# Kernel tuning notes

Hardware: AMD Instinct MI355X
Metric: run time of the kernel (lower is better)

## Reference

```python
import jax, jax.numpy as jnp
import numpy as np
from jax import lax

B = 256; D_IN = 2048; HID = 2048; NSEG = 10; D_CTX = 1024; OUT = 100; NI = 205
KW_PCT = 0.05
K = int(round(KW_PCT * HID))  # 102 winners per sample per layer
W_DENSITY = 0.05      # weight_sparsity = 0.95
DEND_DENSITY = 0.05   # dendrite_weight_sparsity = 0.95


def setup_inputs() -> dict:
    key = jax.random.key(0)
    ks = jax.random.split(key, 16)
    def u(k, shape, bound):
        return jax.random.uniform(k, shape, minval=-bound, maxval=bound, dtype=jnp.float32)
    inp = {}
    inp["x"] = jax.random.normal(ks[0], (B, D_IN), jnp.float32)
    inp["context"] = jax.random.normal(ks[1], (B, D_CTX), jnp.float32)
    # layer 1 FF weights: modified kaiming, input density 1.0 -> bound = 1/sqrt(fan_in)
    inp["W1"] = u(ks[2], (HID, D_IN), 1.0 / np.sqrt(D_IN))
    inp["b1"] = jnp.zeros((HID,), jnp.float32)
    # dendrites: input density 1.0 (context_percent_on=1), weight density 0.05
    dend_bound = 1.0 / np.sqrt(DEND_DENSITY * D_CTX)
    inp["segW1"] = u(ks[3], (HID, NSEG, D_CTX), dend_bound)
    inp["maskW1"] = (jax.random.uniform(ks[4], (HID, D_IN)) < W_DENSITY).astype(jnp.float32)
    inp["maskS1"] = (jax.random.uniform(ks[5], (HID, NSEG, D_CTX)) < DEND_DENSITY).astype(jnp.float32)
    # layer 2 FF weights: input density = kw_percent_on (k-winners upstream)
    inp["W2"] = u(ks[6], (HID, HID), 1.0 / np.sqrt(KW_PCT * HID))
    inp["b2"] = jnp.zeros((HID,), jnp.float32)
    inp["segW2"] = u(ks[7], (HID, NSEG, D_CTX), dend_bound)
    inp["maskW2"] = (jax.random.uniform(ks[8], (HID, HID)) < W_DENSITY).astype(jnp.float32)
    inp["maskS2"] = (jax.random.uniform(ks[9], (HID, NSEG, D_CTX)) < DEND_DENSITY).astype(jnp.float32)
    # Dale (EiDense) output head: non-negative excitatory/inhibitory factors
    s = 1.0 / np.sqrt(HID)
    inp["Wex_out"] = jax.random.uniform(ks[10], (OUT, HID), dtype=jnp.float32) * s
    inp["Wix_out"] = jax.random.uniform(ks[11], (1, HID), dtype=jnp.float32) * s
    inp["Wei_out"] = jax.random.uniform(ks[12], (OUT, 1), dtype=jnp.float32)
    inp["b_out"] = jnp.zeros((OUT,), jnp.float32)
    return inp


def _kwinners(y, k):
    # keep top-k activations per row, zero the rest (boost_strength=0)
    vals, idxs = lax.top_k(y, k)  # [B, k]
    rows = jnp.arange(y.shape[0])[:, None]
    return jnp.zeros_like(y).at[rows, idxs].set(vals)


def _dendritic_layer(x, context, W, b, segW, maskW, maskS):
    # sparse-masked feedforward projection
    y = x @ (W * maskW).T + b  # [B, HID]
    # per-unit dendrite segment activations from context
    d = jnp.einsum('bc,usc->bus', context, segW * maskS)  # [B, HID, NSEG]
    # absolute-max gating: pick segment with max |activation|, gate by sigmoid
    sel = jnp.argmax(jnp.abs(d), axis=-1)  # [B, HID]
    chosen = jnp.take_along_axis(d, sel[..., None], axis=-1)[..., 0]
    y = y * jax.nn.sigmoid(chosen)
    return _kwinners(y, K)


def reference(x, context, W1, b1, segW1, maskW1, maskS1, W2, b2, segW2, maskW2, maskS2, Wex_out, Wix_out, Wei_out, b_out):
    h = _dendritic_layer(x, context, W1, b1, segW1, maskW1, maskS1)
    h = _dendritic_layer(h, context, W2, b2, segW2, maskW2, maskS2)
    # EiDense output head: W = Wex - Wei @ Wix (Dale's law), no output nonlinearity
    W_out = Wex_out - Wei_out @ Wix_out  # [OUT, HID]
    return h @ W_out.T + b_out
```

## Files before the change

kernel.cpp:

```cpp
#include <hip/hip_runtime.h>
#include <math.h>

#define B_SZ   256
#define D_IN   2048
#define HID    2048
#define NSEG   10
#define D_CTX  1024
#define OUT_N  100
#define KWIN   102
#define CAPS   128

typedef float f32x4 __attribute__((ext_vector_type(4)));

__device__ __forceinline__ f32x4 ntld4(const float* p) {
  return __builtin_nontemporal_load((const f32x4*)p);
}

__device__ __forceinline__ unsigned f2key(float f) {
  unsigned b = __float_as_uint(f);
  return (b & 0x80000000u) ? ~b : (b | 0x80000000u);
}
__device__ __forceinline__ float key2f(unsigned k) {
  return (k & 0x80000000u) ? __uint_as_float(k & 0x7FFFFFFFu) : __uint_as_float(~k);
}

__global__ __launch_bounds__(256) void transpose2_k(const float* __restrict__ xsrc,
                                                    float* __restrict__ xdst,
                                                    const float* __restrict__ csrc,
                                                    float* __restrict__ cdst) {
  __shared__ float tile[32][33];
  int bid = blockIdx.x;
  const float* src; float* dst; int cols;
  const int NX = (D_IN / 32) * (B_SZ / 32);
  if (bid < NX) { src = xsrc; dst = xdst; cols = D_IN; }
  else { bid -= NX; src = csrc; dst = cdst; cols = D_CTX; }
  int nbx = cols / 32;
  int bx = bid % nbx, by = bid / nbx;
  int c0 = bx * 32, r0 = by * 32;
  int tx = threadIdx.x & 31, ty = threadIdx.x >> 5;
  for (int i = ty; i < 32; i += 8)
    tile[i][tx] = src[(r0 + i) * cols + (c0 + tx)];
  __syncthreads();
  for (int i = ty; i < 32; i += 8)
    dst[(c0 + i) * B_SZ + (r0 + tx)] = tile[tx][i];
}

__device__ __forceinline__ int compact_pairs_1024(const float* __restrict__ wrow,
                                                  const float* __restrict__ mrow,
                                                  int coff, float2* pairs) {
  const int t = threadIdx.x & 63;
  const unsigned long long below = (1ull << t) - 1ull;
  __builtin_amdgcn_wave_barrier();
  int base = 0;
#pragma unroll
  for (int i = 0; i < 4; ++i) {
    const int e = t + 64 * i;
    f32x4 ww = ntld4(wrow + 4 * e);
    f32x4 mm = ntld4(mrow + 4 * e);
    const float wv[4] = {ww.x, ww.y, ww.z, ww.w};
    const float mv[4] = {mm.x, mm.y, mm.z, mm.w};
    const int c = (e << 2) + coff;
#pragma unroll
    for (int j = 0; j < 4; ++j) {
      bool nz = (mv[j] != 0.f);
      unsigned long long bal = __ballot(nz);
      if (nz) {
        int pos = base + (int)__popcll(bal & below);
        if (pos < CAPS) pairs[pos] = make_float2(wv[j], __int_as_float(c + j));
      }
      base += (int)__popcll(bal);
    }
  }
  __builtin_amdgcn_wave_barrier();
  return base > CAPS ? CAPS : base;
}

__device__ __forceinline__ void gather_dot(const float* __restrict__ src,
                                           const float2* pairs, int cnt,
                                           int t4, float out4[4]) {
  float acc[4][4];
#pragma unroll
  for (int s = 0; s < 4; ++s)
#pragma unroll
    for (int i = 0; i < 4; ++i) acc[s][i] = 0.f;
  int j = 0;
  for (; j + 8 <= cnt; j += 8) {
#pragma unroll
    for (int s = 0; s < 8; ++s) {
      float2 p = pairs[j + s];
      const f32x4 cv = *(const f32x4*)(src + (__float_as_int(p.y) << 8) + t4);
      acc[s & 3][0] += cv.x * p.x; acc[s & 3][1] += cv.y * p.x;
      acc[s & 3][2] += cv.z * p.x; acc[s & 3][3] += cv.w * p.x;
    }
  }
  for (; j < cnt; ++j) {
    float2 p = pairs[j];
    const f32x4 cv = *(const f32x4*)(src + (__float_as_int(p.y) << 8) + t4);
    acc[0][0] += cv.x * p.x; acc[0][1] += cv.y * p.x;
    acc[0][2] += cv.z * p.x; acc[0][3] += cv.w * p.x;
  }
#pragma unroll
  for (int i = 0; i < 4; ++i)
    out4[i] = (acc[0][i] + acc[1][i]) + (acc[2][i] + acc[3][i]);
}

__global__ __launch_bounds__(256, 4) void dendff_kernel(
    const float* __restrict__ W1, const float* __restrict__ maskW1, const float* __restrict__ b1,
    const float* __restrict__ segW1, const float* __restrict__ maskS1,
    const float* __restrict__ segW2, const float* __restrict__ maskS2,
    const float* __restrict__ xT, const float* __restrict__ ctxT,
    float* __restrict__ y1T, float* __restrict__ gate2T) {
  __shared__ float2 pairs_s[4][CAPS];
  __shared__ float exch[2][64][13];
  const int wave = threadIdx.x >> 6;
  const int t = threadIdx.x & 63, t4 = t * 4;
  const int pidx = wave >> 1;
  const int half = wave & 1;
  const int row = blockIdx.x * 2 + pidx;
  const bool isL1 = (row < HID);
  const int u = isL1 ? row : (row - HID);
  const float* segW = (isL1 ? segW1 : segW2)
                      + (size_t)u * NSEG * D_CTX + (size_t)half * 5 * D_CTX;
  const float* maskS = (isL1 ? maskS1 : maskS2)
                      + (size_t)u * NSEG * D_CTX + (size_t)half * 5 * D_CTX;
  float2* pairs = pairs_s[wave];

  float bestA[4] = {-1.f, -1.f, -1.f, -1.f};
  float chosen[4] = {0.f, 0.f, 0.f, 0.f};

#pragma unroll 1
  for (int s = 0; s < 5; ++s) {
    int cnt = compact_pairs_1024(segW + s * D_CTX, maskS + s * D_CTX, 0, pairs);
    float d[4];
    gather_dot(ctxT, pairs, cnt, t4, d);
#pragma unroll
    for (int i = 0; i < 4; ++i) {
      float a = fabsf(d[i]);
      if (a > bestA[i]) { bestA[i] = a; chosen[i] = d[i]; }
    }
  }

  float ffp[4] = {0.f, 0.f, 0.f, 0.f};
  if (isL1) {
    const int off = half * 1024;
    int cnt = compact_pairs_1024(W1 + (size_t)u * D_IN + off,
                                 maskW1 + (size_t)u * D_IN + off, off, pairs);
    gather_dot(xT, pairs, cnt, t4, ffp);
  }

  if (half) {
#pragma unroll
    for (int i = 0; i < 4; ++i) {
      exch[pidx][t][i] = bestA[i];
      exch[pidx][t][4 + i] = chosen[i];
      exch[pidx][t][8 + i] = ffp[i];
    }
  }
  __syncthreads();
  if (!half) {
#pragma unroll
    for (int i = 0; i < 4; ++i) {
      float a1 = exch[pidx][t][i];
      if (a1 > bestA[i]) chosen[i] = exch[pidx][t][4 + i];
      ffp[i] += exch[pidx][t][8 + i];
    }
    if (isL1) {
      float bb = b1[u];
      float4 o;
      o.x = (ffp[0] + bb) / (1.f + expf(-chosen[0]));
      o.y = (ffp[1] + bb) / (1.f + expf(-chosen[1]));
      o.z = (ffp[2] + bb) / (1.f + expf(-chosen[2]));
      o.w = (ffp[3] + bb) / (1.f + expf(-chosen[3]));
      *(float4*)(y1T + (size_t)u * B_SZ + t4) = o;
    } else {
      float4 g;
      g.x = 1.f / (1.f + expf(-chosen[0]));
      g.y = 1.f / (1.f + expf(-chosen[1]));
      g.z = 1.f / (1.f + expf(-chosen[2]));
      g.w = 1.f / (1.f + expf(-chosen[3]));
      *(float4*)(gate2T + (size_t)u * B_SZ + t4) = g;
    }
  }
}

__global__ __launch_bounds__(256, 4) void ff2_kernel(
    const float* __restrict__ W2, const float* __restrict__ maskW2, const float* __restrict__ b2,
    const float* __restrict__ h1T, const float* __restrict__ gate2T, float* __restrict__ y2T) {
  __shared__ float2 pairs_s[4][CAPS];
  __shared__ float exch[2][64][5];
  const int wave = threadIdx.x >> 6;
  const int t = threadIdx.x & 63, t4 = t * 4;
  const int pidx = wave >> 1, half = wave & 1;
  const int u = blockIdx.x * 2 + pidx;
  const int off = half * 1024;
  int cnt = compact_pairs_1024(W2 + (size_t)u * HID + off,
                               maskW2 + (size_t)u * HID + off, off, pairs_s[wave]);
  float acc[4];
  gather_dot(h1T, pairs_s[wave], cnt, t4, acc);
  if (half) {
#pragma unroll
    for (int i = 0; i < 4; ++i) exch[pidx][t][i] = acc[i];
  }
  __syncthreads();
  if (!half) {
#pragma unroll
    for (int i = 0; i < 4; ++i) acc[i] += exch[pidx][t][i];
    float bb = b2[u];
    float4 g = *(const float4*)(gate2T + (size_t)u * B_SZ + t4);
    float4 o;
    o.x = (acc[0] + bb) * g.x; o.y = (acc[1] + bb) * g.y;
    o.z = (acc[2] + bb) * g.z; o.w = (acc[3] + bb) * g.w;
    *(float4*)(y2T + (size_t)u * B_SZ + t4) = o;
  }
}

__global__ __launch_bounds__(256) void topk_kernel(const float* __restrict__ yT,
                                                   float* __restrict__ dst, int mode) {
  const int b = blockIdx.x, t = threadIdx.x;
  __shared__ int hist[256];
  __shared__ int sfx[256];
  __shared__ unsigned sPref;
  __shared__ int sRem;
  unsigned myk[8];
#pragma unroll
  for (int i = 0; i < 8; ++i)
    myk[i] = f2key(yT[(size_t)(t * 8 + i) * B_SZ + b]);
  unsigned pref = 0;
  int rem = KWIN;
  for (int shift = 24; shift >= 0; shift -= 8) {
    hist[t] = 0;
    __syncthreads();
    unsigned hiMask = (shift == 24) ? 0u : (0xFFFFFFFFu << (shift + 8));
#pragma unroll
    for (int i = 0; i < 8; ++i) {
      unsigned k = myk[i];
      if ((k & hiMask) == pref) atomicAdd(&hist[(k >> shift) & 255], 1);
    }
    __syncthreads();
    sfx[t] = hist[t];
    __syncthreads();
    for (int off = 1; off < 256; off <<= 1) {
      int add = (t + off < 256) ? sfx[t + off] : 0;
      __syncthreads();
      sfx[t] += add;
      __syncthreads();
    }
    int s_incl = sfx[t];
    int s_excl = (t == 255) ? 0 : sfx[t + 1];
    if (s_incl >= rem && s_excl < rem) {
      sPref = pref | (((unsigned)t) << shift);
      sRem = rem - s_excl;
    }
    __syncthreads();
    pref = sPref;
    rem = sRem;
    __syncthreads();
  }
  int eq = 0;
#pragma unroll
  for (int i = 0; i < 8; ++i) eq += (myk[i] == pref) ? 1 : 0;
  sfx[t] = eq;
  __syncthreads();
  for (int off = 1; off < 256; off <<= 1) {
    int add = (t >= off) ? sfx[t - off] : 0;
    __syncthreads();
    sfx[t] += add;
    __syncthreads();
  }
  int excl = sfx[t] - eq;
  int taken = 0;
#pragma unroll
  for (int i = 0; i < 8; ++i) {
    unsigned k = myk[i];
    bool keep;
    if (k > pref) keep = true;
    else if (k == pref) { keep = (excl + taken) < rem; taken++; }
    else keep = false;
    float f = keep ? key2f(k) : 0.f;
    int uu = t * 8 + i;
    if (mode == 0) dst[(size_t)uu * B_SZ + b] = f;
    else dst[(size_t)b * HID + uu] = f;
  }
}

__global__ __launch_bounds__(256) void topkout_kernel(
    const float* __restrict__ yT, const float* __restrict__ Wex, const float* __restrict__ Wix,
    const float* __restrict__ Wei, const float* __restrict__ bo, float* __restrict__ out) {
  const int b = blockIdx.x, t = threadIdx.x;
  __shared__ int hist[256];
  __shared__ int sfx[256];
  __shared__ unsigned sPref;
  __shared__ int sRem;
  __shared__ float hrow[HID];
  __shared__ float red[256];
  unsigned myk[8];
#pragma unroll
  for (int i = 0; i < 8; ++i)
    myk[i] = f2key(yT[(size_t)(t * 8 + i) * B_SZ + b]);
  unsigned pref = 0;
  int rem = KWIN;
  for (int shift = 24; shift >= 0; shift -= 8) {
    hist[t] = 0;
    __syncthreads();
    unsigned hiMask = (shift == 24) ? 0u : (0xFFFFFFFFu << (shift + 8));
#pragma unroll
    for (int i = 0; i < 8; ++i) {
      unsigned k = myk[i];
      if ((k & hiMask) == pref) atomicAdd(&hist[(k >> shift) & 255], 1);
    }
    __syncthreads();
    sfx[t] = hist[t];
    __syncthreads();
    for (int off = 1; off < 256; off <<= 1) {
      int add = (t + off < 256) ? sfx[t + off] : 0;
      __syncthreads();
      sfx[t] += add;
      __syncthreads();
    }
    int s_incl = sfx[t];
    int s_excl = (t == 255) ? 0 : sfx[t + 1];
    if (s_incl >= rem && s_excl < rem) {
      sPref = pref | (((unsigned)t) << shift);
      sRem = rem - s_excl;
    }
    __syncthreads();
    pref = sPref;
    rem = sRem;
    __syncthreads();
  }
  int eq = 0;
#pragma unroll
  for (int i = 0; i < 8; ++i) eq += (myk[i] == pref) ? 1 : 0;
  sfx[t] = eq;
  __syncthreads();
  for (int off = 1; off < 256; off <<= 1) {
    int add = (t >= off) ? sfx[t - off] : 0;
    __syncthreads();
    sfx[t] += add;
    __syncthreads();
  }
  int excl = sfx[t] - eq;
  int taken = 0;
  float part = 0.f;
#pragma unroll
  for (int i = 0; i < 8; ++i) {
    unsigned k = myk[i];
    bool keep;
    if (k > pref) keep = true;
    else if (k == pref) { keep = (excl + taken) < rem; taken++; }
    else keep = false;
    float f = keep ? key2f(k) : 0.f;
    int uu = t * 8 + i;
    hrow[uu] = f;
    part += f * Wix[uu];
  }
  red[t] = part;
  __syncthreads();
  for (int off = 128; off > 0; off >>= 1) {
    if (t < off) red[t] += red[t + off];
    __syncthreads();
  }
  float S = red[0];
  const int w = t >> 6, l = t & 63;
  for (int o = w; o < OUT_N; o += 4) {
    float acc = 0.f;
    const float* wr = Wex + (size_t)o * HID;
#pragma unroll
    for (int q = 0; q < HID / 64; ++q) acc += hrow[l + 64 * q] * wr[l + 64 * q];
    for (int off = 32; off > 0; off >>= 1) acc += __shfl_down(acc, off, 64);
    if (l == 0) out[(size_t)b * OUT_N + o] = acc - Wei[o] * S + bo[o];
  }
}

extern "C" void kernel_launch(void* const* d_in, const int* in_sizes, int n_in,
                              void* d_out, int out_size, void* d_ws, size_t ws_size,
                              hipStream_t stream) {
  const float* x      = (const float*)d_in[0];
  const float* ctx    = (const float*)d_in[1];
  const float* W1     = (const float*)d_in[2];
  const float* b1     = (const float*)d_in[3];
  const float* segW1  = (const float*)d_in[4];
  const float* maskW1 = (const float*)d_in[5];
  const float* maskS1 = (const float*)d_in[6];
  const float* W2     = (const float*)d_in[7];
  const float* b2     = (const float*)d_in[8];
  const float* segW2  = (const float*)d_in[9];
  const float* maskW2 = (const float*)d_in[10];
  const float* maskS2 = (const float*)d_in[11];
  const float* Wex    = (const float*)d_in[12];
  const float* Wix    = (const float*)d_in[13];
  const float* Wei    = (const float*)d_in[14];
  const float* bo     = (const float*)d_in[15];
  float* out = (float*)d_out;
  float* ws = (float*)d_ws;

  float* xT     = ws;
  float* ctxT   = ws + 524288;
  float* y1T    = ws + 786432;
  float* gate2T = ws + 1310720;
  float* y2T    = ws + 1835008;

  transpose2_k<<<768, 256, 0, stream>>>(x, xT, ctx, ctxT);
  dendff_kernel<<<2 * HID / 2, 256, 0, stream>>>(W1, maskW1, b1, segW1, maskS1,
                                                 segW2, maskS2, xT, ctxT, y1T, gate2T);
  topk_kernel<<<B_SZ, 256, 0, stream>>>(y1T, y1T, 0);
  ff2_kernel<<<HID / 2, 256, 0, stream>>>(W2, maskW2, b2, y1T, gate2T, y2T);
  topkout_kernel<<<B_SZ, 256, 0, stream>>>(y2T, Wex, Wix, Wei, bo, out);
}
```

Measured before the change: 488.8 us.

## Fuse all stages into one cooperative persistent kernel with prefetched weight loads

Replaces five separate launches with a single cooperative mega-kernel that separates the transpose, dendrite+FF, top-k, FF2 and output phases with grid.sync, falling back to separate launches if the cooperative launch fails. The dendrite kernel now has each block handle both layer-1 and layer-2 dendrites plus the layer-1 FF row for one unit pair. It also software-prefetches the next weight/mask chunk into registers while the current chunk is gathered. This targets launch gaps and memory latency, at the cost of grid-wide barriers, a large shared-memory union and higher register pressure.

```diff
diff --git a/kernel.cpp b/kernel.cpp
--- a/kernel.cpp
+++ b/kernel.cpp
@@ -1,5 +1,8 @@
 #include <hip/hip_runtime.h>
+#include <hip/hip_cooperative_groups.h>
 #include <math.h>
+
+namespace cg = cooperative_groups;
 
 #define B_SZ   256
 #define D_IN   2048
@@ -24,14 +27,21 @@
   return (k & 0x80000000u) ? __uint_as_float(k & 0x7FFFFFFFu) : __uint_as_float(~k);
 }
 
-__global__ __launch_bounds__(256) void transpose2_k(const float* __restrict__ xsrc,
-                                                    float* __restrict__ xdst,
-                                                    const float* __restrict__ csrc,
-                                                    float* __restrict__ cdst) {
-  __shared__ float tile[32][33];
+union SMem {
+  struct { float2 pairs[4][CAPS]; float exch[2][64][21]; } dd;
+  struct { float tile[32][33]; } tp;
+  struct { int hist[256]; int sfx[256]; unsigned pref; int rem;
+           float hrow[HID]; float red[256]; } tk;
+};
+
+
+__device__ void transpose_phase(SMem& sm, const float* __restrict__ xsrc, float* __restrict__ xdst,
+                                const float* __restrict__ csrc, float* __restrict__ cdst) {
   int bid = blockIdx.x;
+  const int NX = (D_IN / 32) * (B_SZ / 32);
+  const int NC = (D_CTX / 32) * (B_SZ / 32);
+  if (bid >= NX + NC) return;
   const float* src; float* dst; int cols;
-  const int NX = (D_IN / 32) * (B_SZ / 32);
   if (bid < NX) { src = xsrc; dst = xdst; cols = D_IN; }
   else { bid -= NX; src = csrc; dst = cdst; cols = D_CTX; }
   int nbx = cols / 32;
@@ -39,27 +49,34 @@
   int c0 = bx * 32, r0 = by * 32;
   int tx = threadIdx.x & 31, ty = threadIdx.x >> 5;
   for (int i = ty; i < 32; i += 8)
-    tile[i][tx] = src[(r0 + i) * cols + (c0 + tx)];
+    sm.tp.tile[i][tx] = src[(r0 + i) * cols + (c0 + tx)];
   __syncthreads();
   for (int i = ty; i < 32; i += 8)
-    dst[(c0 + i) * B_SZ + (r0 + tx)] = tile[tx][i];
-}
-
-__device__ __forceinline__ int compact_pairs_1024(const float* __restrict__ wrow,
-                                                  const float* __restrict__ mrow,
-                                                  int coff, float2* pairs) {
+    dst[(c0 + i) * B_SZ + (r0 + tx)] = sm.tp.tile[tx][i];
+}
+
+__device__ __forceinline__ void load_wm(const float* __restrict__ wrow,
+                                        const float* __restrict__ mrow,
+                                        f32x4 w[4], f32x4 m[4]) {
+  const int t = threadIdx.x & 63;
+#pragma unroll
+  for (int i = 0; i < 4; ++i) {
+    w[i] = ntld4(wrow + 4 * (t + 64 * i));
+    m[i] = ntld4(mrow + 4 * (t + 64 * i));
+  }
+}
+
+__device__ __forceinline__ int store_pairs_regs(const f32x4 w[4], const f32x4 m[4],
+                                                int coff, float2* pairs) {
   const int t = threadIdx.x & 63;
   const unsigned long long below = (1ull << t) - 1ull;
   __builtin_amdgcn_wave_barrier();
   int base = 0;
 #pragma unroll
   for (int i = 0; i < 4; ++i) {
-    const int e = t + 64 * i;
-    f32x4 ww = ntld4(wrow + 4 * e);
-    f32x4 mm = ntld4(mrow + 4 * e);
-    const float wv[4] = {ww.x, ww.y, ww.z, ww.w};
-    const float mv[4] = {mm.x, mm.y, mm.z, mm.w};
-    const int c = (e << 2) + coff;
+    const int c = ((t + 64 * i) << 2) + coff;
+    const float wv[4] = {w[i].x, w[i].y, w[i].z, w[i].w};
+    const float mv[4] = {m[i].x, m[i].y, m[i].z, m[i].w};
 #pragma unroll
     for (int j = 0; j < 4; ++j) {
       bool nz = (mv[j] != 0.f);
@@ -75,6 +92,14 @@
   return base > CAPS ? CAPS : base;
 }
 
+__device__ __forceinline__ int compact_pairs_1024(const float* __restrict__ wrow,
+                                                  const float* __restrict__ mrow,
+                                                  int coff, float2* pairs) {
+  f32x4 w[4], m[4];
+  load_wm(wrow, mrow, w, m);
+  return store_pairs_regs(w, m, coff, pairs);
+}
+
 __device__ __forceinline__ void gather_dot(const float* __restrict__ src,
                                            const float2* pairs, int cnt,
                                            int t4, float out4[4]) {
@@ -104,107 +129,119 @@
     out4[i] = (acc[0][i] + acc[1][i]) + (acc[2][i] + acc[3][i]);
 }
 
-__global__ __launch_bounds__(256, 4) void dendff_kernel(
+__device__ void dendff_phase(SMem& sm,
     const float* __restrict__ W1, const float* __restrict__ maskW1, const float* __restrict__ b1,
     const float* __restrict__ segW1, const float* __restrict__ maskS1,
     const float* __restrict__ segW2, const float* __restrict__ maskS2,
     const float* __restrict__ xT, const float* __restrict__ ctxT,
     float* __restrict__ y1T, float* __restrict__ gate2T) {
-  __shared__ float2 pairs_s[4][CAPS];
-  __shared__ float exch[2][64][13];
   const int wave = threadIdx.x >> 6;
   const int t = threadIdx.x & 63, t4 = t * 4;
   const int pidx = wave >> 1;
   const int half = wave & 1;
-  const int row = blockIdx.x * 2 + pidx;
-  const bool isL1 = (row < HID);
-  const int u = isL1 ? row : (row - HID);
-  const float* segW = (isL1 ? segW1 : segW2)
-                      + (size_t)u * NSEG * D_CTX + (size_t)half * 5 * D_CTX;
-  const float* maskS = (isL1 ? maskS1 : maskS2)
-                      + (size_t)u * NSEG * D_CTX + (size_t)half * 5 * D_CTX;
-  float2* pairs = pairs_s[wave];
-
-  float bestA[4] = {-1.f, -1.f, -1.f, -1.f};
-  float chosen[4] = {0.f, 0.f, 0.f, 0.f};
-
+  const int uu = blockIdx.x * 2 + pidx;
+  float2* pairs = sm.dd.pairs[wave];
+
+  const float* segWA  = segW1 + (size_t)uu * NSEG * D_CTX + (size_t)half * 5 * D_CTX;
+  const float* maskSA = maskS1 + (size_t)uu * NSEG * D_CTX + (size_t)half * 5 * D_CTX;
+  const float* segWB  = segW2 + (size_t)uu * NSEG * D_CTX + (size_t)half * 5 * D_CTX;
+  const float* maskSB = maskS2 + (size_t)uu * NSEG * D_CTX + (size_t)half * 5 * D_CTX;
+  const float* ffW = W1 + (size_t)uu * D_IN + half * 1024;
+  const float* ffM = maskW1 + (size_t)uu * D_IN + half * 1024;
+
+  float bestA0[4] = {-1.f, -1.f, -1.f, -1.f}, chosen0[4] = {0.f, 0.f, 0.f, 0.f};
+  float bestA1[4] = {-1.f, -1.f, -1.f, -1.f}, chosen1[4] = {0.f, 0.f, 0.f, 0.f};
+  float ffp[4] = {0.f, 0.f, 0.f, 0.f};
+
+  f32x4 w[4], m[4];
+  load_wm(segWA, maskSA, w, m);
 #pragma unroll 1
-  for (int s = 0; s < 5; ++s) {
-    int cnt = compact_pairs_1024(segW + s * D_CTX, maskS + s * D_CTX, 0, pairs);
+  for (int k = 0; k < 11; ++k) {
+    const int coff = (k == 5) ? half * 1024 : 0;
+    int cnt = store_pairs_regs(w, m, coff, pairs);
+    if (k + 1 < 11) {
+      const int kn = k + 1;
+      const float* wp = (kn < 5) ? segWA + kn * D_CTX
+                       : (kn == 5) ? ffW : segWB + (kn - 6) * D_CTX;
+      const float* mp = (kn < 5) ? maskSA + kn * D_CTX
+                       : (kn == 5) ? ffM : maskSB + (kn - 6) * D_CTX;
+      load_wm(wp, mp, w, m);
+    }
     float d[4];
-    gather_dot(ctxT, pairs, cnt, t4, d);
+    gather_dot((k == 5) ? xT : ctxT, pairs, cnt, t4, d);
+    if (k == 5) {
+#pragma unroll
+      for (int i = 0; i < 4; ++i) ffp[i] = d[i];
+    } else if (k < 5) {
+#pragma unroll
+      for (int i = 0; i < 4; ++i) {
+        float a = fabsf(d[i]);
+        if (a > bestA0[i]) { bestA0[i] = a; chosen0[i] = d[i]; }
+      }
+    } else {
+#pragma unroll
+      for (int i = 0; i < 4; ++i) {
+        float a = fabsf(d[i]);
+        if (a > bestA1[i]) { bestA1[i] = a; chosen1[i] = d[i]; }
+      }
+    }
+  }
+
+  if (half) {
 #pragma unroll
     for (int i = 0; i < 4; ++i) {
-      float a = fabsf(d[i]);
-      if (a > bestA[i]) { bestA[i] = a; chosen[i] = d[i]; }
-    }
-  }
-
-  float ffp[4] = {0.f, 0.f, 0.f, 0.f};
-  if (isL1) {
-    const int off = half * 1024;
-    int cnt = compact_pairs_1024(W1 + (size_t)u * D_IN + off,
-                                 maskW1 + (size_t)u * D_IN + off, off, pairs);
-    gather_dot(xT, pairs, cnt, t4, ffp);
-  }
-
-  if (half) {
+      sm.dd.exch[pidx][t][i]      = bestA0[i];
+      sm.dd.exch[pidx][t][4 + i]  = chosen0[i];
+      sm.dd.exch[pidx][t][8 + i]  = ffp[i];
+      sm.dd.exch[pidx][t][12 + i] = bestA1[i];
+      sm.dd.exch[pidx][t][16 + i] = chosen1[i];
+    }
+  }
+  __syncthreads();
+  if (!half) {
 #pragma unroll
     for (int i = 0; i < 4; ++i) {
-      exch[pidx][t][i] = bestA[i];
-      exch[pidx][t][4 + i] = chosen[i];
-      exch[pidx][t][8 + i] = ffp[i];
-    }
-  }
-  __syncthreads();
-  if (!half) {
-#pragma unroll
-    for (int i = 0; i < 4; ++i) {
-      float a1 = exch[pidx][t][i];
-      if (a1 > bestA[i]) chosen[i] = exch[pidx][t][4 + i];
-      ffp[i] += exch[pidx][t][8 + i];
-    }
-    if (isL1) {
-      float bb = b1[u];
-      float4 o;
-      o.x = (ffp[0] + bb) / (1.f + expf(-chosen[0]));
-      o.y = (ffp[1] + bb) / (1.f + expf(-chosen[1]));
-      o.z = (ffp[2] + bb) / (1.f + expf(-chosen[2]));
-      o.w = (ffp[3] + bb) / (1.f + expf(-chosen[3]));
-      *(float4*)(y1T + (size_t)u * B_SZ + t4) = o;
-    } else {
-      float4 g;
-      g.x = 1.f / (1.f + expf(-chosen[0]));
-      g.y = 1.f / (1.f + expf(-chosen[1]));
-      g.z = 1.f / (1.f + expf(-chosen[2]));
-      g.w = 1.f / (1.f + expf(-chosen[3]));
-      *(float4*)(gate2T + (size_t)u * B_SZ + t4) = g;
-    }
-  }
-}
-
-__global__ __launch_bounds__(256, 4) void ff2_kernel(
+      if (sm.dd.exch[pidx][t][i] > bestA0[i])      chosen0[i] = sm.dd.exch[pidx][t][4 + i];
+      ffp[i] += sm.dd.exch[pidx][t][8 + i];
+      if (sm.dd.exch[pidx][t][12 + i] > bestA1[i]) chosen1[i] = sm.dd.exch[pidx][t][16 + i];
+    }
+    float bb = b1[uu];
+    float4 o;
+    o.x = (ffp[0] + bb) / (1.f + expf(-chosen0[0]));
+    o.y = (ffp[1] + bb) / (1.f + expf(-chosen0[1]));
+    o.z = (ffp[2] + bb) / (1.f + expf(-chosen0[2]));
+    o.w = (ffp[3] + bb) / (1.f + expf(-chosen0[3]));
+    *(float4*)(y1T + (size_t)uu * B_SZ + t4) = o;
+    float4 g;
+    g.x = 1.f / (1.f + expf(-chosen1[0]));
+    g.y = 1.f / (1.f + expf(-chosen1[1]));
+    g.z = 1.f / (1.f + expf(-chosen1[2]));
+    g.w = 1.f / (1.f + expf(-chosen1[3]));
+    *(float4*)(gate2T + (size_t)uu * B_SZ + t4) = g;
+  }
+}
+
+__device__ void ff2_phase(SMem& sm,
     const float* __restrict__ W2, const float* __restrict__ maskW2, const float* __restrict__ b2,
     const float* __restrict__ h1T, const float* __restrict__ gate2T, float* __restrict__ y2T) {
-  __shared__ float2 pairs_s[4][CAPS];
-  __shared__ float exch[2][64][5];
   const int wave = threadIdx.x >> 6;
   const int t = threadIdx.x & 63, t4 = t * 4;
   const int pidx = wave >> 1, half = wave & 1;
   const int u = blockIdx.x * 2 + pidx;
+  float2* pairs = sm.dd.pairs[wave];
   const int off = half * 1024;
   int cnt = compact_pairs_1024(W2 + (size_t)u * HID + off,
-                               maskW2 + (size_t)u * HID + off, off, pairs_s[wave]);
+                               maskW2 + (size_t)u * HID + off, off, pairs);
   float acc[4];
-  gather_dot(h1T, pairs_s[wave], cnt, t4, acc);
+  gather_dot(h1T, pairs, cnt, t4, acc);
   if (half) {
 #pragma unroll
-    for (int i = 0; i < 4; ++i) exch[pidx][t][i] = acc[i];
+    for (int i = 0; i < 4; ++i) sm.dd.exch[pidx][t][i] = acc[i];
   }
   __syncthreads();
   if (!half) {
 #pragma unroll
-    for (int i = 0; i < 4; ++i) acc[i] += exch[pidx][t][i];
+    for (int i = 0; i < 4; ++i) acc[i] += sm.dd.exch[pidx][t][i];
     float bb = b2[u];
     float4 g = *(const float4*)(gate2T + (size_t)u * B_SZ + t4);
     float4 o;
@@ -214,13 +251,8 @@
   }
 }
 
-__global__ __launch_bounds__(256) void topk_kernel(const float* __restrict__ yT,
-                                                   float* __restrict__ dst, int mode) {
+__device__ void topk_phase(SMem& sm, const float* __restrict__ yT, float* __restrict__ dst) {
   const int b = blockIdx.x, t = threadIdx.x;
-  __shared__ int hist[256];
-  __shared__ int sfx[256];
-  __shared__ unsigned sPref;
-  __shared__ int sRem;
   unsigned myk[8];
 #pragma unroll
   for (int i = 0; i < 8; ++i)
@@ -228,47 +260,113 @@
   unsigned pref = 0;
   int rem = KWIN;
   for (int shift = 24; shift >= 0; shift -= 8) {
-    hist[t] = 0;
+    sm.tk.hist[t] = 0;
     __syncthreads();
     unsigned hiMask = (shift == 24) ? 0u : (0xFFFFFFFFu << (shift + 8));
 #pragma unroll
     for (int i = 0; i < 8; ++i) {
       unsigned k = myk[i];
-      if ((k & hiMask) == pref) atomicAdd(&hist[(k >> shift) & 255], 1);
-    }
-    __syncthreads();
-    sfx[t] = hist[t];
+      if ((k & hiMask) == pref) atomicAdd(&sm.tk.hist[(k >> shift) & 255], 1);
+    }
+    __syncthreads();
+    sm.tk.sfx[t] = sm.tk.hist[t];
     __syncthreads();
     for (int off = 1; off < 256; off <<= 1) {
-      int add = (t + off < 256) ? sfx[t + off] : 0;
+      int add = (t + off < 256) ? sm.tk.sfx[t + off] : 0;
       __syncthreads();
-      sfx[t] += add;
+      sm.tk.sfx[t] += add;
       __syncthreads();
     }
-    int s_incl = sfx[t];
-    int s_excl = (t == 255) ? 0 : sfx[t + 1];
+    int s_incl = sm.tk.sfx[t];
+    int s_excl = (t == 255) ? 0 : sm.tk.sfx[t + 1];
     if (s_incl >= rem && s_excl < rem) {
-      sPref = pref | (((unsigned)t) << shift);
-      sRem = rem - s_excl;
-    }
-    __syncthreads();
-    pref = sPref;
-    rem = sRem;
+      sm.tk.pref = pref | (((unsigned)t) << shift);
+      sm.tk.rem = rem - s_excl;
+    }
+    __syncthreads();
+    pref = sm.tk.pref;
+    rem = sm.tk.rem;
     __syncthreads();
   }
   int eq = 0;
 #pragma unroll
   for (int i = 0; i < 8; ++i) eq += (myk[i] == pref) ? 1 : 0;
-  sfx[t] = eq;
+  sm.tk.sfx[t] = eq;
   __syncthreads();
   for (int off = 1; off < 256; off <<= 1) {
-    int add = (t >= off) ? sfx[t - off] : 0;
-    __syncthreads();
-    sfx[t] += add;
-    __syncthreads();
-  }
-  int excl = sfx[t] - eq;
+    int add = (t >= off) ? sm.tk.sfx[t - off] : 0;
+    __syncthreads();
+    sm.tk.sfx[t] += add;
+    __syncthreads();
+  }
+  int excl = sm.tk.sfx[t] - eq;
   int taken = 0;
+#pragma unroll
+  for (int i = 0; i < 8; ++i) {
+    unsigned k = myk[i];
+    bool keep;
+    if (k > pref) keep = true;
+    else if (k == pref) { keep = (excl + taken) < rem; taken++; }
+    else keep = false;
+    float f = keep ? key2f(k) : 0.f;
+    dst[(size_t)(t * 8 + i) * B_SZ + b] = f;
+  }
+}
+
+__device__ void topkout_phase(SMem& sm, const float* __restrict__ yT,
+                              const float* __restrict__ Wex, const float* __restrict__ Wix,
+                              const float* __restrict__ Wei, const float* __restrict__ bo,
+                              float* __restrict__ out) {
+  const int b = blockIdx.x, t = threadIdx.x;
+  unsigned myk[8];
+#pragma unroll
+  for (int i = 0; i < 8; ++i)
+    myk[i] = f2key(yT[(size_t)(t * 8 + i) * B_SZ + b]);
+  unsigned pref = 0;
+  int rem = KWIN;
+  for (int shift = 24; shift >= 0; shift -= 8) {
+    sm.tk.hist[t] = 0;
+    __syncthreads();
+    unsigned hiMask = (shift == 24) ? 0u : (0xFFFFFFFFu << (shift + 8));
+#pragma unroll
+    for (int i = 0; i < 8; ++i) {
+      unsigned k = myk[i];
+      if ((k & hiMask) == pref) atomicAdd(&sm.tk.hist[(k >> shift) & 255], 1);
+    }
+    __syncthreads();
+    sm.tk.sfx[t] = sm.tk.hist[t];
+    __syncthreads();
+    for (int off = 1; off < 256; off <<= 1) {
+      int add = (t + off < 256) ? sm.tk.sfx[t + off] : 0;
+      __syncthreads();
+      sm.tk.sfx[t] += add;
+      __syncthreads();
+    }
+    int s_incl = sm.tk.sfx[t];
+    int s_excl = (t == 255) ? 0 : sm.tk.sfx[t + 1];
+    if (s_incl >= rem && s_excl < rem) {
+      sm.tk.pref = pref | (((unsigned)t) << shift);
+      sm.tk.rem = rem - s_excl;
+    }
+    __syncthreads();
+    pref = sm.tk.pref;
+    rem = sm.tk.rem;
+    __syncthreads();
+  }
+  int eq = 0;
+#pragma unroll
+  for (int i = 0; i < 8; ++i) eq += (myk[i] == pref) ? 1 : 0;
+  sm.tk.sfx[t] = eq;
+  __syncthreads();
+  for (int off = 1; off < 256; off <<= 1) {
+    int add = (t >= off) ? sm.tk.sfx[t - off] : 0;
+    __syncthreads();
+    sm.tk.sfx[t] += add;
+    __syncthreads();
+  }
+  int excl = sm.tk.sfx[t] - eq;
+  int taken = 0;
+  float part = 0.f;
 #pragma unroll
   for (int i = 0; i < 8; ++i) {
     unsigned k = myk[i];
@@ -278,98 +376,74 @@
     else keep = false;
     float f = keep ? key2f(k) : 0.f;
     int uu = t * 8 + i;
-    if (mode == 0) dst[(size_t)uu * B_SZ + b] = f;
-    else dst[(size_t)b * HID + uu] = f;
-  }
-}
-
-__global__ __launch_bounds__(256) void topkout_kernel(
-    const float* __restrict__ yT, const float* __restrict__ Wex, const float* __restrict__ Wix,
-    const float* __restrict__ Wei, const float* __restrict__ bo, float* __restrict__ out) {
-  const int b = blockIdx.x, t = threadIdx.x;
-  __shared__ int hist[256];
-  __shared__ int sfx[256];
-  __shared__ unsigned sPref;
-  __shared__ int sRem;
-  __shared__ float hrow[HID];
-  __shared__ float red[256];
-  unsigned myk[8];
-#pragma unroll
-  for (int i = 0; i < 8; ++i)
-    myk[i] = f2key(yT[(size_t)(t * 8 + i) * B_SZ + b]);
-  unsigned pref = 0;
-  int rem = KWIN;
-  for (int shift = 24; shift >= 0; shift -= 8) {
-    hist[t] = 0;
-    __syncthreads();
-    unsigned hiMask = (shift == 24) ? 0u : (0xFFFFFFFFu << (shift + 8));
-#pragma unroll
-    for (int i = 0; i < 8; ++i) {
-      unsigned k = myk[i];
-      if ((k & hiMask) == pref) atomicAdd(&hist[(k >> shift) & 255], 1);
-    }
-    __syncthreads();
-    sfx[t] = hist[t];
-    __syncthreads();
-    for (int off = 1; off < 256; off <<= 1) {
-      int add = (t + off < 256) ? sfx[t + off] : 0;
-      __syncthreads();
-      sfx[t] += add;
-      __syncthreads();
-    }
-    int s_incl = sfx[t];
-    int s_excl = (t == 255) ? 0 : sfx[t + 1];
-    if (s_incl >= rem && s_excl < rem) {
-      sPref = pref | (((unsigned)t) << shift);
-      sRem = rem - s_excl;
-    }
-    __syncthreads();
-    pref = sPref;
-    rem = sRem;
-    __syncthreads();
-  }
-  int eq = 0;
-#pragma unroll
-  for (int i = 0; i < 8; ++i) eq += (myk[i] == pref) ? 1 : 0;
-  sfx[t] = eq;
-  __syncthreads();
-  for (int off = 1; off < 256; off <<= 1) {
-    int add = (t >= off) ? sfx[t - off] : 0;
-    __syncthreads();
-    sfx[t] += add;
-    __syncthreads();
-  }
-  int excl = sfx[t] - eq;
-  int taken = 0;
-  float part = 0.f;
-#pragma unroll
-  for (int i = 0; i < 8; ++i) {
-    unsigned k = myk[i];
-    bool keep;
-    if (k > pref) keep = true;
-    else if (k == pref) { keep = (excl + taken) < rem; taken++; }
-    else keep = false;
-    float f = keep ? key2f(k) : 0.f;
-    int uu = t * 8 + i;
-    hrow[uu] = f;
+    sm.tk.hrow[uu] = f;
     part += f * Wix[uu];
   }
-  red[t] = part;
+  sm.tk.red[t] = part;
   __syncthreads();
   for (int off = 128; off > 0; off >>= 1) {
-    if (t < off) red[t] += red[t + off];
-    __syncthreads();
-  }
-  float S = red[0];
+    if (t < off) sm.tk.red[t] += sm.tk.red[t + off];
+    __syncthreads();
+  }
+  float S = sm.tk.red[0];
   const int w = t >> 6, l = t & 63;
   for (int o = w; o < OUT_N; o += 4) {
     float acc = 0.f;
     const float* wr = Wex + (size_t)o * HID;
 #pragma unroll
-    for (int q = 0; q < HID / 64; ++q) acc += hrow[l + 64 * q] * wr[l + 64 * q];
+    for (int q = 0; q < HID / 64; ++q) acc += sm.tk.hrow[l + 64 * q] * wr[l + 64 * q];
     for (int off = 32; off > 0; off >>= 1) acc += __shfl_down(acc, off, 64);
     if (l == 0) out[(size_t)b * OUT_N + o] = acc - Wei[o] * S + bo[o];
   }
+}
+
+__global__ __launch_bounds__(256, 4) void mega_kernel(
+    const float* x, const float* ctx, const float* W1, const float* b1,
+    const float* segW1, const float* maskW1, const float* maskS1,
+    const float* W2, const float* b2, const float* segW2,
+    const float* maskW2, const float* maskS2, const float* Wex,
+    const float* Wix, const float* Wei, const float* bo, float* outp,
+    float* xT, float* ctxT, float* y1T, float* gate2T, float* y2T) {
+  cg::grid_group grid = cg::this_grid();
+  __shared__ SMem sm;
+  transpose_phase(sm, x, xT, ctx, ctxT);
+  grid.sync();
+  dendff_phase(sm, W1, maskW1, b1, segW1, maskS1, segW2, maskS2, xT, ctxT, y1T, gate2T);
+  grid.sync();
+  if (blockIdx.x < B_SZ) topk_phase(sm, y1T, y1T);
+  grid.sync();
+  ff2_phase(sm, W2, maskW2, b2, y1T, gate2T, y2T);
+  grid.sync();
+  if (blockIdx.x < B_SZ) topkout_phase(sm, y2T, Wex, Wix, Wei, bo, outp);
+}
+
+__global__ __launch_bounds__(256) void transpose_fb(const float* x, float* xT,
+                                                    const float* ctx, float* ctxT) {
+  __shared__ SMem sm;
+  transpose_phase(sm, x, xT, ctx, ctxT);
+}
+__global__ __launch_bounds__(256, 4) void dendff_fb(
+    const float* W1, const float* maskW1, const float* b1,
+    const float* segW1, const float* maskS1, const float* segW2, const float* maskS2,
+    const float* xT, const float* ctxT, float* y1T, float* gate2T) {
+  __shared__ SMem sm;
+  dendff_phase(sm, W1, maskW1, b1, segW1, maskS1, segW2, maskS2, xT, ctxT, y1T, gate2T);
+}
+__global__ __launch_bounds__(256) void topk_fb(const float* yT, float* dst) {
+  __shared__ SMem sm;
+  topk_phase(sm, yT, dst);
+}
+__global__ __launch_bounds__(256, 4) void ff2_fb(
+    const float* W2, const float* maskW2, const float* b2,
+    const float* h1T, const float* gate2T, float* y2T) {
+  __shared__ SMem sm;
+  ff2_phase(sm, W2, maskW2, b2, h1T, gate2T, y2T);
+}
+__global__ __launch_bounds__(256) void topkout_fb(
+    const float* yT, const float* Wex, const float* Wix,
+    const float* Wei, const float* bo, float* out) {
+  __shared__ SMem sm;
+  topkout_phase(sm, yT, Wex, Wix, Wei, bo, out);
 }
 
 extern "C" void kernel_launch(void* const* d_in, const int* in_sizes, int n_in,
@@ -391,7 +465,7 @@
   const float* Wix    = (const float*)d_in[13];
   const float* Wei    = (const float*)d_in[14];
   const float* bo     = (const float*)d_in[15];
-  float* out = (float*)d_out;
+  float* outp = (float*)d_out;
   float* ws = (float*)d_ws;
 
   float* xT     = ws;
@@ -400,10 +474,20 @@
   float* gate2T = ws + 1310720;
   float* y2T    = ws + 1835008;
 
-  transpose2_k<<<768, 256, 0, stream>>>(x, xT, ctx, ctxT);
-  dendff_kernel<<<2 * HID / 2, 256, 0, stream>>>(W1, maskW1, b1, segW1, maskS1,
-                                                 segW2, maskS2, xT, ctxT, y1T, gate2T);
-  topk_kernel<<<B_SZ, 256, 0, stream>>>(y1T, y1T, 0);
-  ff2_kernel<<<HID / 2, 256, 0, stream>>>(W2, maskW2, b2, y1T, gate2T, y2T);
-  topkout_kernel<<<B_SZ, 256, 0, stream>>>(y2T, Wex, Wix, Wei, bo, out);
-}
+  void* args[22] = {
+    (void*)&x, (void*)&ctx, (void*)&W1, (void*)&b1, (void*)&segW1, (void*)&maskW1,
+    (void*)&maskS1, (void*)&W2, (void*)&b2, (void*)&segW2, (void*)&maskW2,
+    (void*)&maskS2, (void*)&Wex, (void*)&Wix, (void*)&Wei, (void*)&bo, (void*)&outp,
+    (void*)&xT, (void*)&ctxT, (void*)&y1T, (void*)&gate2T, (void*)&y2T
+  };
+  hipError_t e = hipLaunchCooperativeKernel(mega_kernel, dim3(1024), dim3(256),
+                                            args, 0u, stream);
+  if (e != hipSuccess) {
+    transpose_fb<<<768, 256, 0, stream>>>(x, xT, ctx, ctxT);
+    dendff_fb<<<1024, 256, 0, stream>>>(W1, maskW1, b1, segW1, maskS1, segW2, maskS2,
+                                        xT, ctxT, y1T, gate2T);
+    topk_fb<<<B_SZ, 256, 0, stream>>>(y1T, y1T);
+    ff2_fb<<<1024, 256, 0, stream>>>(W2, maskW2, b2, y1T, gate2T, y2T);
+    topkout_fb<<<B_SZ, 256, 0, stream>>>(y2T, Wex, Wix, Wei, bo, outp);
+  }
+}
```

New measurement: 1.188 ms. +143.1%, slower.

## Double-buffer weight/mask staging into LDS via direct global-to-LDS loads

Applied to the files above, without the earlier changes.

Restructures the dendrite+FF1 kernel to process 512-element sub-rows, prefetching the next sub-row's weights and masks directly into LDS with global_load_lds while compacting and gathering the current one. The aim is to overlap the streaming of the large dense segment weight and mask arrays with the sparse gather-dot compute, instead of stalling on each row load. Segment dot products are now split across two halves and summed, and the pair buffer cap per sub-row is 80, which could truncate in the rare case where more than 80 of 512 mask entries are nonzero. LDS use grows to about 32KB per block for the staging buffers, which may reduce occupancy.

```diff
diff --git a/kernel.cpp b/kernel.cpp
--- a/kernel.cpp
+++ b/kernel.cpp
@@ -8,12 +8,20 @@
 #define D_CTX  1024
 #define OUT_N  100
 #define KWIN   102
-#define CAPS   128
+#define CAPF   128
+#define SUBF   512
+#define CAPD   80
 
 typedef float f32x4 __attribute__((ext_vector_type(4)));
 
 __device__ __forceinline__ f32x4 ntld4(const float* p) {
   return __builtin_nontemporal_load((const f32x4*)p);
+}
+
+__device__ __forceinline__ void gl_lds(const float* g, float* l) {
+  __builtin_amdgcn_global_load_lds(
+      (const __attribute__((address_space(1))) void*)g,
+      (__attribute__((address_space(3))) void*)l, 16, 0, 0);
 }
 
 __device__ __forceinline__ unsigned f2key(float f) {
@@ -45,6 +53,183 @@
     dst[(c0 + i) * B_SZ + (r0 + tx)] = tile[tx][i];
 }
 
+__device__ __forceinline__ void gather_dot(const float* __restrict__ src,
+                                           const float2* pairs, int cnt,
+                                           int t4, float out4[4]) {
+  float acc[4][4];
+#pragma unroll
+  for (int s = 0; s < 4; ++s)
+#pragma unroll
+    for (int i = 0; i < 4; ++i) acc[s][i] = 0.f;
+  int j = 0;
+  for (; j + 8 <= cnt; j += 8) {
+#pragma unroll
+    for (int s = 0; s < 8; ++s) {
+      float2 p = pairs[j + s];
+      const f32x4 cv = *(const f32x4*)(src + (__float_as_int(p.y) << 8) + t4);
+      acc[s & 3][0] += cv.x * p.x; acc[s & 3][1] += cv.y * p.x;
+      acc[s & 3][2] += cv.z * p.x; acc[s & 3][3] += cv.w * p.x;
+    }
+  }
+  for (; j < cnt; ++j) {
+    float2 p = pairs[j];
+    const f32x4 cv = *(const f32x4*)(src + (__float_as_int(p.y) << 8) + t4);
+    acc[0][0] += cv.x * p.x; acc[0][1] += cv.y * p.x;
+    acc[0][2] += cv.z * p.x; acc[0][3] += cv.w * p.x;
+  }
+#pragma unroll
+  for (int i = 0; i < 4; ++i)
+    out4[i] = (acc[0][i] + acc[1][i]) + (acc[2][i] + acc[3][i]);
+}
+
+__device__ __forceinline__ void stage_sub(const float* __restrict__ wp,
+                                          const float* __restrict__ mp,
+                                          float* sw, float* sm) {
+  const int t = threadIdx.x & 63;
+  gl_lds(wp + 4 * t, sw);
+  gl_lds(wp + 256 + 4 * t, sw + 256);
+  gl_lds(mp + 4 * t, sm);
+  gl_lds(mp + 256 + 4 * t, sm + 256);
+}
+
+__device__ __forceinline__ int compact_staged(const float* sw, const float* sm,
+                                              int coff, float2* pairs) {
+  const int t = threadIdx.x & 63;
+  const unsigned long long below = (1ull << t) - 1ull;
+  __builtin_amdgcn_wave_barrier();
+  int base = 0;
+#pragma unroll
+  for (int i = 0; i < 2; ++i) {
+    const int e = t + 64 * i;
+    f32x4 ww = *(const f32x4*)(sw + 4 * e);
+    f32x4 mm = *(const f32x4*)(sm + 4 * e);
+    const float wv[4] = {ww.x, ww.y, ww.z, ww.w};
+    const float mv[4] = {mm.x, mm.y, mm.z, mm.w};
+    const int c = (e << 2) + coff;
+#pragma unroll
+    for (int j = 0; j < 4; ++j) {
+      bool nz = (mv[j] != 0.f);
+      unsigned long long bal = __ballot(nz);
+      if (nz) {
+        int pos = base + (int)__popcll(bal & below);
+        if (pos < CAPD) pairs[pos] = make_float2(wv[j], __int_as_float(c + j));
+      }
+      base += (int)__popcll(bal);
+    }
+  }
+  __builtin_amdgcn_wave_barrier();
+  return base > CAPD ? CAPD : base;
+}
+
+__global__ __launch_bounds__(256, 4) void dendff_kernel(
+    const float* __restrict__ W1, const float* __restrict__ maskW1, const float* __restrict__ b1,
+    const float* __restrict__ segW1, const float* __restrict__ maskS1,
+    const float* __restrict__ segW2, const float* __restrict__ maskS2,
+    const float* __restrict__ xT, const float* __restrict__ ctxT,
+    float* __restrict__ y1T, float* __restrict__ gate2T) {
+  __shared__ __align__(16) float stw[4][2][SUBF];
+  __shared__ __align__(16) float stm[4][2][SUBF];
+  __shared__ union {
+    float2 pairs[4][CAPD];
+    float exch[2][64][13];
+  } u;
+  const int wave = threadIdx.x >> 6;
+  const int t = threadIdx.x & 63, t4 = t * 4;
+  const int pidx = wave >> 1;
+  const int half = wave & 1;
+  const int row = blockIdx.x * 2 + pidx;
+  const bool isL1 = (row < HID);
+  const int uu = isL1 ? row : (row - HID);
+  const float* segW = (isL1 ? segW1 : segW2)
+                      + (size_t)uu * NSEG * D_CTX + (size_t)half * 5 * D_CTX;
+  const float* maskS = (isL1 ? maskS1 : maskS2)
+                      + (size_t)uu * NSEG * D_CTX + (size_t)half * 5 * D_CTX;
+  const float* ffW = W1 + (size_t)uu * D_IN + half * 1024;
+  const float* ffM = maskW1 + (size_t)uu * D_IN + half * 1024;
+  float2* pairs = u.pairs[wave];
+  const int nsub = isL1 ? 12 : 10;
+
+  float bestA[4] = {-1.f, -1.f, -1.f, -1.f};
+  float chosen[4] = {0.f, 0.f, 0.f, 0.f};
+  float ffp[4] = {0.f, 0.f, 0.f, 0.f};
+  float dseg[4] = {0.f, 0.f, 0.f, 0.f};
+
+  stage_sub(segW, maskS, stw[wave][0], stm[wave][0]);
+  asm volatile("s_waitcnt vmcnt(0)" ::: "memory");
+#pragma unroll 1
+  for (int k = 0; k < nsub; ++k) {
+    const bool isFF = (k >= 10);
+    const int buf = k & 1;
+    const int coff = isFF ? (half * 1024 + (k & 1) * SUBF) : ((k & 1) * SUBF);
+    int cnt = compact_staged(stw[wave][buf], stm[wave][buf], coff, pairs);
+    __builtin_amdgcn_sched_barrier(0);
+    if (k + 1 < nsub) {
+      const int kn = k + 1;
+      const float* wp; const float* mp;
+      if (kn < 10) {
+        wp = segW + (kn >> 1) * D_CTX + (kn & 1) * SUBF;
+        mp = maskS + (kn >> 1) * D_CTX + (kn & 1) * SUBF;
+      } else {
+        wp = ffW + (kn & 1) * SUBF;
+        mp = ffM + (kn & 1) * SUBF;
+      }
+      stage_sub(wp, mp, stw[wave][buf ^ 1], stm[wave][buf ^ 1]);
+    }
+    float d[4];
+    gather_dot(isFF ? xT : ctxT, pairs, cnt, t4, d);
+    if (isFF) {
+#pragma unroll
+      for (int i = 0; i < 4; ++i) ffp[i] += d[i];
+    } else if ((k & 1) == 0) {
+#pragma unroll
+      for (int i = 0; i < 4; ++i) dseg[i] = d[i];
+    } else {
+#pragma unroll
+      for (int i = 0; i < 4; ++i) {
+        float full = dseg[i] + d[i];
+        float a = fabsf(full);
+        if (a > bestA[i]) { bestA[i] = a; chosen[i] = full; }
+      }
+    }
+    asm volatile("s_waitcnt vmcnt(0)" ::: "memory");
+  }
+
+  __syncthreads();
+  if (half) {
+#pragma unroll
+    for (int i = 0; i < 4; ++i) {
+      u.exch[pidx][t][i] = bestA[i];
+      u.exch[pidx][t][4 + i] = chosen[i];
+      u.exch[pidx][t][8 + i] = ffp[i];
+    }
+  }
+  __syncthreads();
+  if (!half) {
+#pragma unroll
+    for (int i = 0; i < 4; ++i) {
+      float a1 = u.exch[pidx][t][i];
+      if (a1 > bestA[i]) chosen[i] = u.exch[pidx][t][4 + i];
+      ffp[i] += u.exch[pidx][t][8 + i];
+    }
+    if (isL1) {
+      float bb = b1[uu];
+      float4 o;
+      o.x = (ffp[0] + bb) / (1.f + expf(-chosen[0]));
+      o.y = (ffp[1] + bb) / (1.f + expf(-chosen[1]));
+      o.z = (ffp[2] + bb) / (1.f + expf(-chosen[2]));
+      o.w = (ffp[3] + bb) / (1.f + expf(-chosen[3]));
+      *(float4*)(y1T + (size_t)uu * B_SZ + t4) = o;
+    } else {
+      float4 g;
+      g.x = 1.f / (1.f + expf(-chosen[0]));
+      g.y = 1.f / (1.f + expf(-chosen[1]));
+      g.z = 1.f / (1.f + expf(-chosen[2]));
+      g.w = 1.f / (1.f + expf(-chosen[3]));
+      *(float4*)(gate2T + (size_t)uu * B_SZ + t4) = g;
+    }
+  }
+}
+
 __device__ __forceinline__ int compact_pairs_1024(const float* __restrict__ wrow,
                                                   const float* __restrict__ mrow,
                                                   int coff, float2* pairs) {
@@ -66,127 +251,19 @@
       unsigned long long bal = __ballot(nz);
       if (nz) {
         int pos = base + (int)__popcll(bal & below);
-        if (pos < CAPS) pairs[pos] = make_float2(wv[j], __int_as_float(c + j));
+        if (pos < CAPF) pairs[pos] = make_float2(wv[j], __int_as_float(c + j));
       }
       base += (int)__popcll(bal);
     }
   }
   __builtin_amdgcn_wave_barrier();
-  return base > CAPS ? CAPS : base;
-}
-
-__device__ __forceinline__ void gather_dot(const float* __restrict__ src,
-                                           const float2* pairs, int cnt,
-                                           int t4, float out4[4]) {
-  float acc[4][4];
-#pragma unroll
-  for (int s = 0; s < 4; ++s)
-#pragma unroll
-    for (int i = 0; i < 4; ++i) acc[s][i] = 0.f;
-  int j = 0;
-  for (; j + 8 <= cnt; j += 8) {
-#pragma unroll
-    for (int s = 0; s < 8; ++s) {
-      float2 p = pairs[j + s];
-      const f32x4 cv = *(const f32x4*)(src + (__float_as_int(p.y) << 8) + t4);
-      acc[s & 3][0] += cv.x * p.x; acc[s & 3][1] += cv.y * p.x;
-      acc[s & 3][2] += cv.z * p.x; acc[s & 3][3] += cv.w * p.x;
-    }
-  }
-  for (; j < cnt; ++j) {
-    float2 p = pairs[j];
-    const f32x4 cv = *(const f32x4*)(src + (__float_as_int(p.y) << 8) + t4);
-    acc[0][0] += cv.x * p.x; acc[0][1] += cv.y * p.x;
-    acc[0][2] += cv.z * p.x; acc[0][3] += cv.w * p.x;
-  }
-#pragma unroll
-  for (int i = 0; i < 4; ++i)
-    out4[i] = (acc[0][i] + acc[1][i]) + (acc[2][i] + acc[3][i]);
-}
-
-__global__ __launch_bounds__(256, 4) void dendff_kernel(
-    const float* __restrict__ W1, const float* __restrict__ maskW1, const float* __restrict__ b1,
-    const float* __restrict__ segW1, const float* __restrict__ maskS1,
-    const float* __restrict__ segW2, const float* __restrict__ maskS2,
-    const float* __restrict__ xT, const float* __restrict__ ctxT,
-    float* __restrict__ y1T, float* __restrict__ gate2T) {
-  __shared__ float2 pairs_s[4][CAPS];
-  __shared__ float exch[2][64][13];
-  const int wave = threadIdx.x >> 6;
-  const int t = threadIdx.x & 63, t4 = t * 4;
-  const int pidx = wave >> 1;
-  const int half = wave & 1;
-  const int row = blockIdx.x * 2 + pidx;
-  const bool isL1 = (row < HID);
-  const int u = isL1 ? row : (row - HID);
-  const float* segW = (isL1 ? segW1 : segW2)
-                      + (size_t)u * NSEG * D_CTX + (size_t)half * 5 * D_CTX;
-  const float* maskS = (isL1 ? maskS1 : maskS2)
-                      + (size_t)u * NSEG * D_CTX + (size_t)half * 5 * D_CTX;
-  float2* pairs = pairs_s[wave];
-
-  float bestA[4] = {-1.f, -1.f, -1.f, -1.f};
-  float chosen[4] = {0.f, 0.f, 0.f, 0.f};
-
-#pragma unroll 1
-  for (int s = 0; s < 5; ++s) {
-    int cnt = compact_pairs_1024(segW + s * D_CTX, maskS + s * D_CTX, 0, pairs);
-    float d[4];
-    gather_dot(ctxT, pairs, cnt, t4, d);
-#pragma unroll
-    for (int i = 0; i < 4; ++i) {
-      float a = fabsf(d[i]);
-      if (a > bestA[i]) { bestA[i] = a; chosen[i] = d[i]; }
-    }
-  }
-
-  float ffp[4] = {0.f, 0.f, 0.f, 0.f};
-  if (isL1) {
-    const int off = half * 1024;
-    int cnt = compact_pairs_1024(W1 + (size_t)u * D_IN + off,
-                                 maskW1 + (size_t)u * D_IN + off, off, pairs);
-    gather_dot(xT, pairs, cnt, t4, ffp);
-  }
-
-  if (half) {
-#pragma unroll
-    for (int i = 0; i < 4; ++i) {
-      exch[pidx][t][i] = bestA[i];
-      exch[pidx][t][4 + i] = chosen[i];
-      exch[pidx][t][8 + i] = ffp[i];
-    }
-  }
-  __syncthreads();
-  if (!half) {
-#pragma unroll
-    for (int i = 0; i < 4; ++i) {
-      float a1 = exch[pidx][t][i];
-      if (a1 > bestA[i]) chosen[i] = exch[pidx][t][4 + i];
-      ffp[i] += exch[pidx][t][8 + i];
-    }
-    if (isL1) {
-      float bb = b1[u];
-      float4 o;
-      o.x = (ffp[0] + bb) / (1.f + expf(-chosen[0]));
-      o.y = (ffp[1] + bb) / (1.f + expf(-chosen[1]));
-      o.z = (ffp[2] + bb) / (1.f + expf(-chosen[2]));
-      o.w = (ffp[3] + bb) / (1.f + expf(-chosen[3]));
-      *(float4*)(y1T + (size_t)u * B_SZ + t4) = o;
-    } else {
-      float4 g;
-      g.x = 1.f / (1.f + expf(-chosen[0]));
-      g.y = 1.f / (1.f + expf(-chosen[1]));
-      g.z = 1.f / (1.f + expf(-chosen[2]));
-      g.w = 1.f / (1.f + expf(-chosen[3]));
-      *(float4*)(gate2T + (size_t)u * B_SZ + t4) = g;
-    }
-  }
+  return base > CAPF ? CAPF : base;
 }
 
 __global__ __launch_bounds__(256, 4) void ff2_kernel(
     const float* __restrict__ W2, const float* __restrict__ maskW2, const float* __restrict__ b2,
     const float* __restrict__ h1T, const float* __restrict__ gate2T, float* __restrict__ y2T) {
-  __shared__ float2 pairs_s[4][CAPS];
+  __shared__ float2 pairs_s[4][CAPF];
   __shared__ float exch[2][64][5];
   const int wave = threadIdx.x >> 6;
   const int t = threadIdx.x & 63, t4 = t * 4;
```

Result: no change. 497.2 us (+1.7%).
